# Kernel optimization log

Measured on AMD Instinct MI355X. Metric: run time of the kernel, lower is better.

Reference implementation:

```python
import jax, jax.numpy as jnp
import numpy as np

N = 96            # num_orbitals
C = 128           # hidden_channels
H = 16            # num_heads
D = C // H        # head_dim = 8
LN_EPS = 1e-6


def setup_inputs() -> dict:
    key = jax.random.key(0)
    ks = jax.random.split(key, 10)
    x = jax.random.normal(ks[0], (N, C), dtype=jnp.float32)
    H_core = jax.random.normal(ks[1], (N, N), dtype=jnp.float32)
    X = jax.random.normal(ks[2], (N, N), dtype=jnp.float32)
    eri = jax.random.normal(ks[3], (N, N, N, N), dtype=jnp.float32)
    P_init = jax.random.normal(ks[4], (N, N), dtype=jnp.float32)
    # learned params (flax Dense: kernel [in, out]; LayerNorm scale/bias)
    ln_scale = jnp.ones((C,), dtype=jnp.float32)
    ln_bias = jnp.zeros((C,), dtype=jnp.float32)
    Wqkv = jax.random.normal(ks[5], (C, 3 * C), dtype=jnp.float32) / np.sqrt(C)
    Wout = jax.random.normal(ks[6], (C, C), dtype=jnp.float32) / np.sqrt(C)
    bout = jnp.zeros((C,), dtype=jnp.float32)
    return {"x": x, "H_core": H_core, "X": X, "eri": eri, "P_init": P_init,
            "ln_scale": ln_scale, "ln_bias": ln_bias,
            "Wqkv": Wqkv, "Wout": Wout, "bout": bout}


def reference(x, H_core, X, eri, P_init, ln_scale, ln_bias, Wqkv, Wout, bout):
    # quantum bias terms
    J = jnp.einsum('kl,ijkl->ij', P_init, eri)      # Coulomb
    K = jnp.einsum('ij,ikjl->kl', P_init, eri)      # exchange
    diff_JK = J - K / 2
    L = X @ H_core @ X.T
    # LayerNorm over feature dim
    mu = jnp.mean(x, axis=-1, keepdims=True)
    var = jnp.mean((x - mu) ** 2, axis=-1, keepdims=True)
    xn = (x - mu) * jax.lax.rsqrt(var + LN_EPS) * ln_scale + ln_bias
    # QKV projection (no bias)
    qkv = xn @ Wqkv                                   # [N, 3C]
    q, k, v = jnp.split(qkv, 3, axis=-1)
    q = q.reshape(N, H, D); k = k.reshape(N, H, D); v = v.reshape(N, H, D)
    qk = jnp.einsum('ihd,jhd->hij', q, k) / jnp.sqrt(jnp.float32(D))  # [H,N,N]
    # per-head-slice bias injection
    qk = qk.at[0:2].add(H_core[None])
    qk = qk.at[2:4].add(diff_JK[None])
    qk = qk.at[4:6].add(L[None])
    attn = jax.nn.softmax(qk, axis=-1)
    out = jnp.einsum('hij,jhd->ihd', attn, v).reshape(N, C)
    return out @ Wout + bout
```

## Files before the change

### kernel.cpp

```cpp
#include <hip/hip_runtime.h>

#define NORB 96
#define NN 9216

typedef float f32x4 __attribute__((ext_vector_type(4)));

__global__ __launch_bounds__(192) void prep_kernel(
    const float* __restrict__ X, const float* __restrict__ Hc,
    const float* __restrict__ x, const float* __restrict__ ln_s,
    const float* __restrict__ ln_b, const float* __restrict__ Wqkv,
    float* __restrict__ Lm, float* __restrict__ Km, float* __restrict__ qkv) {
  const int blk = blockIdx.x;
  const int t = threadIdx.x;
  if (blk < 96) {
    const int i = blk;
    __shared__ float Xs[NN];
    __shared__ float tmp[NORB];
    for (int f = t; f < NN; f += 192) Xs[f] = X[f];
    if (t < NORB) Km[i * NORB + t] = 0.f;
    __syncthreads();
    if (t < NORB) {
      float acc = 0.f;
      for (int m = 0; m < NORB; ++m) acc += Xs[i * NORB + m] * Hc[m * NORB + t];
      tmp[t] = acc;
    }
    __syncthreads();
    if (t < NORB) {
      float acc = 0.f;
      for (int k = 0; k < NORB; ++k) acc += tmp[k] * Xs[t * NORB + k];
      Lm[i * NORB + t] = acc;
    }
  } else {
    const int i = blk - 96;
    __shared__ float xn[128];
    __shared__ float red[3];
    float v = (t < 128) ? x[i * 128 + t] : 0.f;
    float s = v;
#pragma unroll
    for (int off = 32; off; off >>= 1) s += __shfl_down(s, off);
    if ((t & 63) == 0) red[t >> 6] = s;
    __syncthreads();
    const float mu = (red[0] + red[1] + red[2]) * (1.f / 128.f);
    __syncthreads();
    const float dv = (t < 128) ? (v - mu) : 0.f;
    s = dv * dv;
#pragma unroll
    for (int off = 32; off; off >>= 1) s += __shfl_down(s, off);
    if ((t & 63) == 0) red[t >> 6] = s;
    __syncthreads();
    const float var = (red[0] + red[1] + red[2]) * (1.f / 128.f);
    if (t < 128) xn[t] = dv * rsqrtf(var + 1e-6f) * ln_s[t] + ln_b[t];
    __syncthreads();
#pragma unroll
    for (int jj = 0; jj < 2; ++jj) {
      const int j = t + jj * 192;
      float acc = 0.f;
      for (int c = 0; c < 128; ++c) acc += xn[c] * Wqkv[c * 384 + j];
      qkv[i * 384 + j] = acc;
    }
  }
}

__global__ __launch_bounds__(384) void jk_kernel(
    const float* __restrict__ eri, const float* __restrict__ P,
    float* __restrict__ Jm, float* __restrict__ Km) {
  const int ab = blockIdx.x;
  const int a = ab / NORB;
  const int b = ab - a * NORB;
  const int t = threadIdx.x;
  const int x = t % 24;
  const int y = t / 24;
  const f32x4* __restrict__ slab4 = (const f32x4*)(eri + (size_t)ab * NN);
  const f32x4* __restrict__ P4 = (const f32x4*)P;

  __shared__ float pa_sh[NORB];
  __shared__ float klp[16][NORB];
  __shared__ float js[6];

  if (t < NORB) pa_sh[t] = P[a * NORB + t];

  f32x4 pvr[6];
#pragma unroll
  for (int k = 0; k < 6; ++k) pvr[k] = P4[t + 384 * k];
  __syncthreads();

  float jp = 0.f, k0 = 0.f, k1 = 0.f, k2 = 0.f, k3 = 0.f;
#pragma unroll
  for (int k = 0; k < 6; ++k) {
    const f32x4 v = __builtin_nontemporal_load(&slab4[t + 384 * k]);
    const float pa = pa_sh[y + 16 * k];
    jp += v.x * pvr[k].x + v.y * pvr[k].y + v.z * pvr[k].z + v.w * pvr[k].w;
    k0 += pa * v.x;
    k1 += pa * v.y;
    k2 += pa * v.z;
    k3 += pa * v.w;
  }

  klp[y][4 * x + 0] = k0;
  klp[y][4 * x + 1] = k1;
  klp[y][4 * x + 2] = k2;
  klp[y][4 * x + 3] = k3;
#pragma unroll
  for (int off = 32; off; off >>= 1) jp += __shfl_down(jp, off);
  if ((t & 63) == 0) js[t >> 6] = jp;
  __syncthreads();
  if (t == 0)
    Jm[ab] = js[0] + js[1] + js[2] + js[3] + js[4] + js[5];
  if (t < NORB) {
    float kk = 0.f;
#pragma unroll
    for (int yy = 0; yy < 16; ++yy) kk += klp[yy][t];
    atomicAdd(&Km[b * NORB + t], kk);
  }
}

__global__ __launch_bounds__(128) void attn_kernel(
    const float* __restrict__ qkv, const float* __restrict__ Hc,
    const float* __restrict__ Jm, const float* __restrict__ Km,
    const float* __restrict__ Lm, float* __restrict__ aout) {
  const int i = blockIdx.x >> 4;
  const int h = blockIdx.x & 15;
  const int t = threadIdx.x;
  __shared__ float q_sh[8];
  __shared__ float p[NORB];
  __shared__ float redm[2];
  __shared__ float reds[2];
  __shared__ float pvred[16][8];

  if (t < 8) q_sh[t] = qkv[i * 384 + h * 8 + t];
  __syncthreads();

  float score = -1e30f;
  if (t < NORB) {
    const float* kr = qkv + t * 384 + 128 + h * 8;
    float d = 0.f;
#pragma unroll
    for (int dd = 0; dd < 8; ++dd) d += q_sh[dd] * kr[dd];
    d *= 0.3535533905932738f;
    const int ij = i * NORB + t;
    if (h < 2) d += Hc[ij];
    else if (h < 4) d += Jm[ij] - 0.5f * Km[ij];
    else if (h < 6) d += Lm[ij];
    score = d;
  }

  float m = score;
#pragma unroll
  for (int off = 32; off; off >>= 1) m = fmaxf(m, __shfl_down(m, off));
  if ((t & 63) == 0) redm[t >> 6] = m;
  __syncthreads();
  m = fmaxf(redm[0], redm[1]);

  float e = (t < NORB) ? __expf(score - m) : 0.f;
  float s = e;
#pragma unroll
  for (int off = 32; off; off >>= 1) s += __shfl_down(s, off);
  if ((t & 63) == 0) reds[t >> 6] = s;
  if (t < NORB) p[t] = e;
  __syncthreads();
  const float denom = reds[0] + reds[1];

  const int dd = t & 7;
  const int g = t >> 3;
  float acc = 0.f;
  for (int j = g; j < NORB; j += 16) acc += p[j] * qkv[j * 384 + 256 + h * 8 + dd];
  pvred[g][dd] = acc;
  __syncthreads();
  if (t < 8) {
    float o = 0.f;
#pragma unroll
    for (int g2 = 0; g2 < 16; ++g2) o += pvred[g2][t];
    aout[i * 128 + h * 8 + t] = o / denom;
  }
}

__global__ __launch_bounds__(128) void out_proj_kernel(
    const float* __restrict__ aout, const float* __restrict__ Wout,
    const float* __restrict__ bout, float* __restrict__ y) {
  const int i = blockIdx.x;
  const int j = threadIdx.x;
  __shared__ float row[128];
  row[j] = aout[i * 128 + j];
  __syncthreads();
  float acc = bout[j];
  for (int c = 0; c < 128; ++c) acc += row[c] * Wout[c * 128 + j];
  y[i * 128 + j] = acc;
}

extern "C" void kernel_launch(void* const* d_in, const int* in_sizes, int n_in,
                              void* d_out, int out_size, void* d_ws,
                              size_t ws_size, hipStream_t stream) {
  const float* x    = (const float*)d_in[0];
  const float* Hc   = (const float*)d_in[1];
  const float* X    = (const float*)d_in[2];
  const float* eri  = (const float*)d_in[3];
  const float* P    = (const float*)d_in[4];
  const float* ln_s = (const float*)d_in[5];
  const float* ln_b = (const float*)d_in[6];
  const float* Wqkv = (const float*)d_in[7];
  const float* Wout = (const float*)d_in[8];
  const float* bout = (const float*)d_in[9];
  float* y = (float*)d_out;

  float* ws   = (float*)d_ws;
  float* Jm   = ws;
  float* Km   = ws + NN;
  float* Lm   = ws + 2 * NN;
  float* qkv  = ws + 3 * NN;
  float* aout = qkv + 96 * 384;

  prep_kernel<<<192, 192, 0, stream>>>(X, Hc, x, ln_s, ln_b, Wqkv, Lm, Km, qkv);

  jk_kernel<<<NN, 384, 0, stream>>>(eri, P, Jm, Km);

  attn_kernel<<<NORB * 16, 128, 0, stream>>>(qkv, Hc, Jm, Km, Lm, aout);

  out_proj_kernel<<<NORB, 128, 0, stream>>>(aout, Wout, bout, y);
}
```

Measured before the change: 73.74 us.

## Process two eri slabs per JK block and fuse attention with output projection

The JK kernel now handles two a-indices per block for the same b. Their exchange contributions are summed in registers before the shared reduction, which halves the atomicAdd traffic to K and doubles the loads in flight per thread. The attention and output-projection kernels are merged into one 256-thread block per row, with all 16 heads' softmax done in-register via 16-lane shuffles. This removes a launch and the aout round trip through global memory, at the cost of fewer blocks (96) in the fused kernel.

```diff
diff --git a/kernel.cpp b/kernel.cpp
--- a/kernel.cpp
+++ b/kernel.cpp
@@ -64,48 +64,62 @@
 __global__ __launch_bounds__(384) void jk_kernel(
     const float* __restrict__ eri, const float* __restrict__ P,
     float* __restrict__ Jm, float* __restrict__ Km) {
-  const int ab = blockIdx.x;
-  const int a = ab / NORB;
-  const int b = ab - a * NORB;
+  const int blk = blockIdx.x;
+  const int b = blk % NORB;
+  const int ap = blk / NORB;
+  const int a0 = 2 * ap, a1 = a0 + 1;
   const int t = threadIdx.x;
   const int x = t % 24;
   const int y = t / 24;
-  const f32x4* __restrict__ slab4 = (const f32x4*)(eri + (size_t)ab * NN);
+  const f32x4* __restrict__ slab0 =
+      (const f32x4*)(eri + (size_t)(a0 * NORB + b) * NN);
+  const f32x4* __restrict__ slab1 =
+      (const f32x4*)(eri + (size_t)(a1 * NORB + b) * NN);
   const f32x4* __restrict__ P4 = (const f32x4*)P;
 
-  __shared__ float pa_sh[NORB];
+  __shared__ float pa_sh[2][NORB];
   __shared__ float klp[16][NORB];
-  __shared__ float js[6];
-
-  if (t < NORB) pa_sh[t] = P[a * NORB + t];
+  __shared__ float js[2][6];
+
+  if (t < NORB) pa_sh[0][t] = P[a0 * NORB + t];
+  else if (t < 2 * NORB) pa_sh[1][t - NORB] = P[a1 * NORB + (t - NORB)];
 
   f32x4 pvr[6];
 #pragma unroll
   for (int k = 0; k < 6; ++k) pvr[k] = P4[t + 384 * k];
   __syncthreads();
 
-  float jp = 0.f, k0 = 0.f, k1 = 0.f, k2 = 0.f, k3 = 0.f;
+  float jp0 = 0.f, jp1 = 0.f;
+  f32x4 kacc = {0.f, 0.f, 0.f, 0.f};
 #pragma unroll
   for (int k = 0; k < 6; ++k) {
-    const f32x4 v = __builtin_nontemporal_load(&slab4[t + 384 * k]);
-    const float pa = pa_sh[y + 16 * k];
-    jp += v.x * pvr[k].x + v.y * pvr[k].y + v.z * pvr[k].z + v.w * pvr[k].w;
-    k0 += pa * v.x;
-    k1 += pa * v.y;
-    k2 += pa * v.z;
-    k3 += pa * v.w;
-  }
-
-  klp[y][4 * x + 0] = k0;
-  klp[y][4 * x + 1] = k1;
-  klp[y][4 * x + 2] = k2;
-  klp[y][4 * x + 3] = k3;
-#pragma unroll
-  for (int off = 32; off; off >>= 1) jp += __shfl_down(jp, off);
-  if ((t & 63) == 0) js[t >> 6] = jp;
-  __syncthreads();
-  if (t == 0)
-    Jm[ab] = js[0] + js[1] + js[2] + js[3] + js[4] + js[5];
+    const f32x4 v0 = __builtin_nontemporal_load(&slab0[t + 384 * k]);
+    const f32x4 v1 = __builtin_nontemporal_load(&slab1[t + 384 * k]);
+    const float pa0 = pa_sh[0][y + 16 * k];
+    const float pa1 = pa_sh[1][y + 16 * k];
+    jp0 += v0.x * pvr[k].x + v0.y * pvr[k].y + v0.z * pvr[k].z + v0.w * pvr[k].w;
+    jp1 += v1.x * pvr[k].x + v1.y * pvr[k].y + v1.z * pvr[k].z + v1.w * pvr[k].w;
+    kacc += pa0 * v0 + pa1 * v1;
+  }
+
+  klp[y][4 * x + 0] = kacc.x;
+  klp[y][4 * x + 1] = kacc.y;
+  klp[y][4 * x + 2] = kacc.z;
+  klp[y][4 * x + 3] = kacc.w;
+#pragma unroll
+  for (int off = 32; off; off >>= 1) {
+    jp0 += __shfl_down(jp0, off);
+    jp1 += __shfl_down(jp1, off);
+  }
+  if ((t & 63) == 0) {
+    js[0][t >> 6] = jp0;
+    js[1][t >> 6] = jp1;
+  }
+  __syncthreads();
+  if (t < 2) {
+    const float* j6 = js[t];
+    Jm[(a0 + t) * NORB + b] = j6[0] + j6[1] + j6[2] + j6[3] + j6[4] + j6[5];
+  }
   if (t < NORB) {
     float kk = 0.f;
 #pragma unroll
@@ -114,77 +128,69 @@
   }
 }
 
-__global__ __launch_bounds__(128) void attn_kernel(
+__global__ __launch_bounds__(256) void attn_proj_kernel(
     const float* __restrict__ qkv, const float* __restrict__ Hc,
     const float* __restrict__ Jm, const float* __restrict__ Km,
-    const float* __restrict__ Lm, float* __restrict__ aout) {
-  const int i = blockIdx.x >> 4;
-  const int h = blockIdx.x & 15;
+    const float* __restrict__ Lm, const float* __restrict__ Wout,
+    const float* __restrict__ bout, float* __restrict__ y) {
+  const int i = blockIdx.x;
   const int t = threadIdx.x;
-  __shared__ float q_sh[8];
-  __shared__ float p[NORB];
-  __shared__ float redm[2];
-  __shared__ float reds[2];
-  __shared__ float pvred[16][8];
-
-  if (t < 8) q_sh[t] = qkv[i * 384 + h * 8 + t];
-  __syncthreads();
-
-  float score = -1e30f;
-  if (t < NORB) {
-    const float* kr = qkv + t * 384 + 128 + h * 8;
+  __shared__ float qs[128];
+  __shared__ float ps[16][97];
+  __shared__ float aout_sh[128];
+
+  if (t < 128) qs[t] = qkv[i * 384 + t];
+  __syncthreads();
+
+  const int h = t >> 4;
+  const int jg = t & 15;
+  float sc[6];
+#pragma unroll
+  for (int m = 0; m < 6; ++m) {
+    const int j = jg + 16 * m;
+    const float* kr = qkv + j * 384 + 128 + h * 8;
     float d = 0.f;
 #pragma unroll
-    for (int dd = 0; dd < 8; ++dd) d += q_sh[dd] * kr[dd];
+    for (int dd = 0; dd < 8; ++dd) d += qs[h * 8 + dd] * kr[dd];
     d *= 0.3535533905932738f;
-    const int ij = i * NORB + t;
+    const int ij = i * NORB + j;
     if (h < 2) d += Hc[ij];
     else if (h < 4) d += Jm[ij] - 0.5f * Km[ij];
     else if (h < 6) d += Lm[ij];
-    score = d;
-  }
-
-  float m = score;
-#pragma unroll
-  for (int off = 32; off; off >>= 1) m = fmaxf(m, __shfl_down(m, off));
-  if ((t & 63) == 0) redm[t >> 6] = m;
-  __syncthreads();
-  m = fmaxf(redm[0], redm[1]);
-
-  float e = (t < NORB) ? __expf(score - m) : 0.f;
-  float s = e;
-#pragma unroll
-  for (int off = 32; off; off >>= 1) s += __shfl_down(s, off);
-  if ((t & 63) == 0) reds[t >> 6] = s;
-  if (t < NORB) p[t] = e;
-  __syncthreads();
-  const float denom = reds[0] + reds[1];
-
-  const int dd = t & 7;
-  const int g = t >> 3;
-  float acc = 0.f;
-  for (int j = g; j < NORB; j += 16) acc += p[j] * qkv[j * 384 + 256 + h * 8 + dd];
-  pvred[g][dd] = acc;
-  __syncthreads();
-  if (t < 8) {
-    float o = 0.f;
-#pragma unroll
-    for (int g2 = 0; g2 < 16; ++g2) o += pvred[g2][t];
-    aout[i * 128 + h * 8 + t] = o / denom;
-  }
-}
-
-__global__ __launch_bounds__(128) void out_proj_kernel(
-    const float* __restrict__ aout, const float* __restrict__ Wout,
-    const float* __restrict__ bout, float* __restrict__ y) {
-  const int i = blockIdx.x;
-  const int j = threadIdx.x;
-  __shared__ float row[128];
-  row[j] = aout[i * 128 + j];
-  __syncthreads();
-  float acc = bout[j];
-  for (int c = 0; c < 128; ++c) acc += row[c] * Wout[c * 128 + j];
-  y[i * 128 + j] = acc;
+    sc[m] = d;
+  }
+  float mx = sc[0];
+#pragma unroll
+  for (int m = 1; m < 6; ++m) mx = fmaxf(mx, sc[m]);
+#pragma unroll
+  for (int off = 8; off; off >>= 1) mx = fmaxf(mx, __shfl_xor(mx, off, 16));
+  float sm = 0.f;
+#pragma unroll
+  for (int m = 0; m < 6; ++m) {
+    sc[m] = __expf(sc[m] - mx);
+    sm += sc[m];
+  }
+#pragma unroll
+  for (int off = 8; off; off >>= 1) sm += __shfl_xor(sm, off, 16);
+  const float inv = 1.f / sm;
+#pragma unroll
+  for (int m = 0; m < 6; ++m) ps[h][jg + 16 * m] = sc[m] * inv;
+  __syncthreads();
+
+  if (t < 128) {
+    const int h2 = t >> 3;
+    float acc = 0.f;
+#pragma unroll 8
+    for (int j = 0; j < NORB; ++j) acc += ps[h2][j] * qkv[j * 384 + 256 + t];
+    aout_sh[t] = acc;
+  }
+  __syncthreads();
+  if (t < 128) {
+    float acc = bout[t];
+#pragma unroll 8
+    for (int c = 0; c < 128; ++c) acc += aout_sh[c] * Wout[c * 128 + t];
+    y[i * 128 + t] = acc;
+  }
 }
 
 extern "C" void kernel_launch(void* const* d_in, const int* in_sizes, int n_in,
@@ -202,18 +208,15 @@
   const float* bout = (const float*)d_in[9];
   float* y = (float*)d_out;
 
-  float* ws   = (float*)d_ws;
-  float* Jm   = ws;
-  float* Km   = ws + NN;
-  float* Lm   = ws + 2 * NN;
-  float* qkv  = ws + 3 * NN;
-  float* aout = qkv + 96 * 384;
+  float* ws  = (float*)d_ws;
+  float* Jm  = ws;
+  float* Km  = ws + NN;
+  float* Lm  = ws + 2 * NN;
+  float* qkv = ws + 3 * NN;
 
   prep_kernel<<<192, 192, 0, stream>>>(X, Hc, x, ln_s, ln_b, Wqkv, Lm, Km, qkv);
 
-  jk_kernel<<<NN, 384, 0, stream>>>(eri, P, Jm, Km);
-
-  attn_kernel<<<NORB * 16, 128, 0, stream>>>(qkv, Hc, Jm, Km, Lm, aout);
-
-  out_proj_kernel<<<NORB, 128, 0, stream>>>(aout, Wout, bout, y);
-}
+  jk_kernel<<<4608, 384, 0, stream>>>(eri, P, Jm, Km);
+
+  attn_proj_kernel<<<NORB, 256, 0, stream>>>(qkv, Hc, Jm, Km, Lm, Wout, bout, y);
+}
```

Measured after the change: 75.12 us. About the same (+1.9%).
